# Kernel optimization log

Measured on AMD Instinct MI355X. Metric: run time of the kernel, lower is better.

## Reference

```python
import jax, jax.numpy as jnp
import numpy as np

B, D_IN, LAT, C = 16384, 512, 64, 8
HID = [1024, 512, 256]

def _lin(k, fi, fo, scale=0.02):
    k1, k2 = jax.random.split(k)
    return jax.random.normal(k1, (fi, fo), jnp.float32) * scale, jax.random.normal(k2, (fo,), jnp.float32) * scale

def _lin_c(k, fi, fo, scale=0.02):
    k1, k2 = jax.random.split(k)
    return jax.random.normal(k1, (C, fi, fo), jnp.float32) * scale, jax.random.normal(k2, (C, fo), jnp.float32) * scale

def setup_inputs() -> dict:
    key = jax.random.key(0)
    ks = jax.random.split(key, 16)
    x = jax.random.normal(ks[0], (B, D_IN), jnp.float32)
    cluster_labels = jax.random.randint(ks[1], (B,), 0, C, jnp.int32)
    eps = jax.random.normal(ks[2], (B, LAT), jnp.float32)
    # encoder: shared(512->1024), unshared(1024->512), shared(512->256)
    enc_W0, enc_b0 = _lin(ks[3], D_IN, HID[0])
    enc_Wu, enc_bu = _lin_c(ks[4], HID[0], HID[1])
    enc_W2, enc_b2 = _lin(ks[5], HID[1], HID[2])
    # shared latent heads
    mu_W, mu_b = _lin(ks[6], HID[2], LAT)
    lv_W, lv_b = _lin(ks[7], HID[2], LAT)
    # decoder (hidden_dims reversed = [256,512,1024]): unshared(64->256), shared(256->512), unshared(512->1024)
    dec_Wu0, dec_bu0 = _lin_c(ks[8], LAT, HID[2])
    dec_W1, dec_b1 = _lin(ks[9], HID[2], HID[1])
    dec_Wu2, dec_bu2 = _lin_c(ks[10], HID[1], HID[0])
    # per-cluster final layer (1024 -> input_dim), no activation (all-continuous)
    fin_W, fin_b = _lin_c(ks[11], HID[0], D_IN)
    return dict(x=x, cluster_labels=cluster_labels, eps=eps,
                enc_W0=enc_W0, enc_b0=enc_b0, enc_Wu=enc_Wu, enc_bu=enc_bu,
                enc_W2=enc_W2, enc_b2=enc_b2, mu_W=mu_W, mu_b=mu_b,
                lv_W=lv_W, lv_b=lv_b, dec_Wu0=dec_Wu0, dec_bu0=dec_bu0,
                dec_W1=dec_W1, dec_b1=dec_b1, dec_Wu2=dec_Wu2, dec_bu2=dec_bu2,
                fin_W=fin_W, fin_b=fin_b)

def _unshared(h, W, b, labels):
    # per-cluster GEMM then row-wise combine (mask-based dispatch, no row reorder)
    y = jnp.einsum('bi,cio->bco', h, W) + b[None]  # [B, C, out]
    return jnp.take_along_axis(y, labels[:, None, None], axis=1)[:, 0, :]

def reference(x, cluster_labels, eps,
              enc_W0, enc_b0, enc_Wu, enc_bu, enc_W2, enc_b2,
              mu_W, mu_b, lv_W, lv_b,
              dec_Wu0, dec_bu0, dec_W1, dec_b1, dec_Wu2, dec_bu2,
              fin_W, fin_b):
    lbl = cluster_labels.astype(jnp.int32)
    # encoder
    h = jax.nn.relu(x @ enc_W0 + enc_b0)
    h = jax.nn.relu(_unshared(h, enc_Wu, enc_bu, lbl))
    h = jax.nn.relu(h @ enc_W2 + enc_b2)
    mu = h @ mu_W + mu_b
    logvar = h @ lv_W + lv_b
    # reparameterize
    z = mu + jnp.exp(0.5 * logvar) * eps
    # decoder
    h = jax.nn.relu(_unshared(z, dec_Wu0, dec_bu0, lbl))
    h = jax.nn.relu(h @ dec_W1 + dec_b1)
    h = jax.nn.relu(_unshared(h, dec_Wu2, dec_bu2, lbl))
    # per-cluster final output layer (identity activation: all-continuous)
    recon = _unshared(h, fin_W, fin_b, lbl)
    return recon
```

## Files before the change

kernel.cpp:

```cpp
#include <hip/hip_runtime.h>

typedef _Float16 f16;
typedef __attribute__((ext_vector_type(8))) _Float16 f16x8;
typedef __attribute__((ext_vector_type(4))) _Float16 f16x4;
typedef __attribute__((ext_vector_type(4))) float    f32x4;

#define B_ROWS 16384
#define MPAD   17408
#define MTILES 136
#define NBLK   64

typedef __attribute__((address_space(1))) void as1_void;
typedef __attribute__((address_space(3))) void as3_void;

__device__ __forceinline__ void gl_lds16(const void* g, void* l) {
    __builtin_amdgcn_global_load_lds((const as1_void*)g, (as3_void*)l, 16, 0, 0);
}


__global__ __launch_bounds__(256) void k_prep(const int* __restrict__ lbl, int* __restrict__ blockhist,
                                              int* __restrict__ rowmap,
                                              const float* __restrict__ mb_, const float* __restrict__ lb_,
                                              float* __restrict__ bz, f16* __restrict__ zerob) {
    int b = blockIdx.x, t = threadIdx.x;
    int i = b * 256 + t;
    rowmap[i] = -1;
    if (b < NBLK) {
        __shared__ int h[8];
        if (t < 8) h[t] = 0;
        __syncthreads();
        atomicAdd(&h[lbl[i]], 1);
        __syncthreads();
        if (t < 8) blockhist[b * 8 + t] = h[t];
    } else if (b == NBLK) {
        if (t < 64) zerob[t] = (f16)0.f;
        if (t < 64) bz[t] = mb_[t];
        else if (t < 128) bz[t] = lb_[t - 64];
    }
}

__global__ void k_offsets(const int* __restrict__ blockhist, int* offs, int* tilec, int* blockbase) {
    __shared__ int tot[8];
    __shared__ int so[9];
    int t = threadIdx.x;
    if (t < 8) {
        int s = 0;
        for (int b = 0; b < NBLK; ++b) s += blockhist[b * 8 + t];
        tot[t] = s;
    }
    __syncthreads();
    if (t == 0) {
        int o = 0;
        for (int c = 0; c < 8; ++c) { so[c] = o; o += (tot[c] + 127) & ~127; }
        so[8] = o;
        for (int c = 0; c < 9; ++c) offs[c] = so[c];
    }
    __syncthreads();
    if (t < 8) {
        int run = so[t];
        for (int b = 0; b < NBLK; ++b) {
            blockbase[b * 8 + t] = run;
            run += blockhist[b * 8 + t];
        }
    }
    if (t < MTILES) {
        int row = t * 128, c = 7;
        for (int cc = 0; cc < 8; ++cc)
            if (row >= so[cc] && row < so[cc + 1]) c = cc;
        tilec[t] = c;
    }
}

__global__ __launch_bounds__(256) void k_scatter(const int* __restrict__ lbl,
                                                 const int* __restrict__ blockbase,
                                                 int* __restrict__ rowmap) {
    __shared__ int cur[8];
    if (threadIdx.x < 8) cur[threadIdx.x] = blockbase[blockIdx.x * 8 + threadIdx.x];
    __syncthreads();
    int i = blockIdx.x * 256 + threadIdx.x;
    int c = lbl[i];
    int pos = atomicAdd(&cur[c], 1);
    rowmap[pos] = i;
}


struct Seg { const float* s; f16* d; int K, N, b0, nx, ny; long sCS, dCS; };
struct SegTab { Seg g[10]; };

__global__ __launch_bounds__(256) void k_trans(SegTab tab, const float* __restrict__ x, f16* __restrict__ xh) {
    int bid = blockIdx.x;
    if (bid < tab.g[1].b0) {
        int i = bid * 256 + threadIdx.x;
        float4 v = ((const float4*)x)[i];
        f16x4 o = {(f16)v.x, (f16)v.y, (f16)v.z, (f16)v.w};
        ((f16x4*)xh)[i] = o;
        return;
    }
    int s = 9;
    while (bid < tab.g[s].b0) --s;
    Seg sg = tab.g[s];
    int lb = bid - sg.b0;
    int nxy = sg.nx * sg.ny;
    int z = lb / nxy; int r = lb - z * nxy;
    int by = r / sg.nx; int bx = r - by * sg.nx;
    const float* src = sg.s + (size_t)z * sg.sCS;
    f16* dst = sg.d + (size_t)z * sg.dCS;
    int n0 = bx * 32, k0 = by * 32;
    int tx = threadIdx.x & 31, ty = threadIdx.x >> 5;
    __shared__ float t[32][33];
    #pragma unroll
    for (int i = 0; i < 32; i += 8)
        t[ty + i][tx] = src[(size_t)(k0 + ty + i) * sg.N + n0 + tx];
    __syncthreads();
    #pragma unroll
    for (int i = 0; i < 32; i += 8)
        dst[(size_t)(n0 + ty + i) * sg.K + k0 + tx] = (f16)t[tx][ty + i];
}

__global__ __launch_bounds__(256) void k_reparam(const f16* __restrict__ muv, const float* __restrict__ eps,
                                                 const int* __restrict__ rowmap, f16* __restrict__ z) {
    int i = blockIdx.x * 256 + threadIdx.x;
    int p = i >> 6, j = i & 63;
    int g = rowmap[p];
    float e  = (g >= 0) ? eps[(size_t)g * 64 + j] : 0.f;
    float mu = (float)muv[(size_t)p * 128 + j];
    float lv = (float)muv[(size_t)p * 128 + 64 + j];
    z[i] = (f16)(mu + expf(0.5f * lv) * e);
}


template<int GATHER, int PERW, int RELU, int SCATTER>
__global__ __launch_bounds__(256) void gemm_k(
    const f16* __restrict__ A, const f16* __restrict__ Wt,
    const float* __restrict__ bias, f16* __restrict__ Out, float* __restrict__ OutF,
    const int* __restrict__ rowmap, const int* __restrict__ tilec,
    const f16* __restrict__ zerobuf, int K, int N)
{
    __shared__ __align__(16) f16 lA[128 * 64];
    __shared__ __align__(16) f16 lB[128 * 64];
    const int tid  = threadIdx.x;
    const int wave = tid >> 6;
    const int lane = tid & 63;

    const int id  = blockIdx.x;
    const int xcd = id & 7;
    const int jj  = id >> 3;
    const int tm  = (jj % 17) * 8 + xcd;
    const int tn  = jj / 17;
    const int r0 = tm * 128, n0 = tn * 128;

    const f16* wb = Wt;
    const float* bb = bias;
    if (PERW) {
        int c = tilec[tm];
        wb += (size_t)c * K * N;
        bb += (size_t)c * N;
    }

    const int srow = tid >> 3;
    const int sg   = tid & 7;
    const int xk16 = (sg ^ (srow & 7)) * 16;
    const size_t rowB = (size_t)K * 2;
    const size_t passB = 32 * rowB;

    const char* pa[4]; size_t stepA[4];
    #pragma unroll
    for (int p = 0; p < 4; ++p) {
        int gr = r0 + p * 32 + srow;
        if (GATHER) {
            int g = rowmap[gr];
            if (g >= 0) { pa[p] = (const char*)(A + (size_t)g * K) + xk16; stepA[p] = 128; }
            else        { pa[p] = (const char*)zerobuf;                    stepA[p] = 0;   }
        } else {
            pa[p] = (const char*)(A + (size_t)gr * K) + xk16; stepA[p] = 128;
        }
    }
    const char* pb = (const char*)(wb + (size_t)(n0 + srow) * K) + xk16;

    const int mb = (wave >> 1) * 64;
    const int nb = (wave & 1) * 64;
    const int quad = lane >> 4;
    const int r16  = lane & 15;
    const int key  = r16 & 7;

    f32x4 acc[4][4];
    #pragma unroll
    for (int i = 0; i < 4; ++i)
        #pragma unroll
        for (int j = 0; j < 4; ++j)
            acc[i][j] = (f32x4){0.f, 0.f, 0.f, 0.f};

    const int nk = K >> 6;
    for (int kb = 0; kb < nk; ++kb) {
        #pragma unroll
        for (int p = 0; p < 4; ++p)
            gl_lds16(pa[p], (char*)lA + p * 4096 + wave * 1024);
        #pragma unroll
        for (int p = 0; p < 4; ++p)
            gl_lds16(pb + p * passB, (char*)lB + p * 4096 + wave * 1024);
        __syncthreads();
        #pragma unroll
        for (int kk = 0; kk < 2; ++kk) {
            const int off = ((kk * 4 + quad) ^ key) * 16;
            f16x8 af[4], bf[4];
            #pragma unroll
            for (int i = 0; i < 4; ++i)
                af[i] = *(const f16x8*)((const char*)lA + (mb + i * 16 + r16) * 128 + off);
            #pragma unroll
            for (int j = 0; j < 4; ++j)
                bf[j] = *(const f16x8*)((const char*)lB + (nb + j * 16 + r16) * 128 + off);
            #pragma unroll
            for (int i = 0; i < 4; ++i)
                #pragma unroll
                for (int j = 0; j < 4; ++j)
                    acc[i][j] = __builtin_amdgcn_mfma_f32_16x16x32_f16(af[i], bf[j], acc[i][j], 0, 0, 0);
        }
        __syncthreads();
        #pragma unroll
        for (int p = 0; p < 4; ++p) pa[p] += stepA[p];
        pb += 128;
    }

    float bv[4];
    #pragma unroll
    for (int j = 0; j < 4; ++j) bv[j] = bb[n0 + nb + j * 16 + r16];

    #pragma unroll
    for (int i = 0; i < 4; ++i) {
        #pragma unroll
        for (int r = 0; r < 4; ++r) {
            int orow = r0 + mb + i * 16 + quad * 4 + r;
            int g = 0;
            if (SCATTER) g = rowmap[orow];
            #pragma unroll
            for (int j = 0; j < 4; ++j) {
                int ocol = n0 + nb + j * 16 + r16;
                float v = acc[i][j][r] + bv[j];
                if (RELU) v = fmaxf(v, 0.f);
                if (SCATTER) {
                    if (g >= 0) OutF[(size_t)g * N + ocol] = v;
                } else {
                    Out[(size_t)orow * N + ocol] = (f16)v;
                }
            }
        }
    }
}


extern "C" void kernel_launch(void* const* d_in, const int* in_sizes, int n_in,
                              void* d_out, int out_size, void* d_ws, size_t ws_size,
                              hipStream_t stream) {
    const float* x      = (const float*)d_in[0];
    const int*   lbl    = (const int*)  d_in[1];
    const float* eps    = (const float*)d_in[2];
    const float* enc_W0 = (const float*)d_in[3];
    const float* enc_b0 = (const float*)d_in[4];
    const float* enc_Wu = (const float*)d_in[5];
    const float* enc_bu = (const float*)d_in[6];
    const float* enc_W2 = (const float*)d_in[7];
    const float* enc_b2 = (const float*)d_in[8];
    const float* mu_W   = (const float*)d_in[9];
    const float* mu_b   = (const float*)d_in[10];
    const float* lv_W   = (const float*)d_in[11];
    const float* lv_b   = (const float*)d_in[12];
    const float* dWu0   = (const float*)d_in[13];
    const float* dbu0   = (const float*)d_in[14];
    const float* dW1    = (const float*)d_in[15];
    const float* db1    = (const float*)d_in[16];
    const float* dWu2   = (const float*)d_in[17];
    const float* dbu2   = (const float*)d_in[18];
    const float* finW   = (const float*)d_in[19];
    const float* finb   = (const float*)d_in[20];
    float* out = (float*)d_out;
    (void)in_sizes; (void)n_in; (void)out_size; (void)ws_size;

    char* base = (char*)d_ws;
    size_t off = 0;
    auto alloc = [&](size_t bytes) { char* r = base + off; off = (off + bytes + 255) & ~(size_t)255; return r; };
    f16* xh     = (f16*)alloc((size_t)B_ROWS * 512 * 2);
    f16* buf1   = (f16*)alloc((size_t)MPAD * 1024 * 2);
    f16* buf2   = (f16*)alloc((size_t)MPAD * 512 * 2);
    f16* buf3   = (f16*)alloc((size_t)MPAD * 256 * 2);
    f16* muv    = (f16*)alloc((size_t)MPAD * 128 * 2);
    f16* zb     = (f16*)alloc((size_t)MPAD * 64 * 2);
    f16* w0t    = (f16*)alloc(1024ul * 512 * 2);
    f16* wut    = (f16*)alloc(8ul * 512 * 1024 * 2);
    f16* w2t    = (f16*)alloc(256ul * 512 * 2);
    f16* wzt    = (f16*)alloc(128ul * 256 * 2);
    f16* wd0t   = (f16*)alloc(8ul * 256 * 64 * 2);
    f16* wd1t   = (f16*)alloc(512ul * 256 * 2);
    f16* wd2t   = (f16*)alloc(8ul * 1024 * 512 * 2);
    f16* wft    = (f16*)alloc(8ul * 512 * 1024 * 2);
    float* bz   = (float*)alloc(128 * 4);
    int* rowmap = (int*)alloc(MPAD * 4);
    int* blockhist = (int*)alloc(NBLK * 8 * 4);
    int* blockbase = (int*)alloc(NBLK * 8 * 4);
    int* offs   = (int*)alloc(64);
    int* tilec  = (int*)alloc(MTILES * 4);
    f16* zerob  = (f16*)alloc(256);

    k_prep<<<MPAD / 256, 256, 0, stream>>>(lbl, blockhist, rowmap, mu_b, lv_b, bz, zerob);
    k_offsets<<<1, 256, 0, stream>>>(blockhist, offs, tilec, blockbase);
    k_scatter<<<NBLK, 256, 0, stream>>>(lbl, blockbase, rowmap);

    SegTab tab;
    int b0 = B_ROWS * 512 / 4 / 256;
    auto seg = [&](int i, const float* s, f16* d, int K, int N, int nz, long sCS, long dCS) {
        int nx = N / 32, ny = K / 32;
        tab.g[i] = Seg{s, d, K, N, b0, nx, ny, sCS, dCS};
        b0 += nx * ny * nz;
    };
    tab.g[0] = Seg{nullptr, nullptr, 0, 0, 0, 0, 0, 0, 0};
    seg(1, enc_W0, w0t, 512, 1024, 1, 0, 0);
    seg(2, enc_Wu, wut, 1024, 512, 8, 1024l * 512, 512l * 1024);
    seg(3, enc_W2, w2t, 512, 256, 1, 0, 0);
    seg(4, mu_W, wzt, 256, 64, 1, 0, 0);
    seg(5, lv_W, wzt + 64 * 256, 256, 64, 1, 0, 0);
    seg(6, dWu0, wd0t, 64, 256, 8, 64l * 256, 256l * 64);
    seg(7, dW1, wd1t, 256, 512, 1, 0, 0);
    seg(8, dWu2, wd2t, 512, 1024, 8, 512l * 1024, 1024l * 512);
    seg(9, finW, wft, 1024, 512, 8, 1024l * 512, 512l * 1024);
    k_trans<<<b0, 256, 0, stream>>>(tab, x, xh);

    gemm_k<1,0,1,0><<<MTILES * 8, 256, 0, stream>>>(xh,   w0t,  enc_b0, buf1, nullptr, rowmap, tilec, zerob, 512, 1024);
    gemm_k<0,1,1,0><<<MTILES * 4, 256, 0, stream>>>(buf1, wut,  enc_bu, buf2, nullptr, rowmap, tilec, zerob, 1024, 512);
    gemm_k<0,0,1,0><<<MTILES * 2, 256, 0, stream>>>(buf2, w2t,  enc_b2, buf3, nullptr, rowmap, tilec, zerob, 512, 256);
    gemm_k<0,0,0,0><<<MTILES * 1, 256, 0, stream>>>(buf3, wzt,  bz,     muv,  nullptr, rowmap, tilec, zerob, 256, 128);
    k_reparam<<<MPAD * 64 / 256, 256, 0, stream>>>(muv, eps, rowmap, zb);
    gemm_k<0,1,1,0><<<MTILES * 2, 256, 0, stream>>>(zb,   wd0t, dbu0,   buf3, nullptr, rowmap, tilec, zerob, 64, 256);
    gemm_k<0,0,1,0><<<MTILES * 4, 256, 0, stream>>>(buf3, wd1t, db1,    buf2, nullptr, rowmap, tilec, zerob, 256, 512);
    gemm_k<0,1,1,0><<<MTILES * 8, 256, 0, stream>>>(buf2, wd2t, dbu2,   buf1, nullptr, rowmap, tilec, zerob, 512, 1024);
    gemm_k<0,1,0,1><<<MTILES * 4, 256, 0, stream>>>(buf1, wft,  finb,   nullptr, out,  rowmap, tilec, zerob, 1024, 512);
}
```

Baseline: 354.3 us.

## Stage GEMM epilogues through LDS for vectorized stores and fuse reparameterization

The GEMM epilogue now writes the accumulator tile into swizzled shared memory and then emits wide 16-byte coalesced stores, replacing per-element scattered 2-byte or 4-byte writes. The final scatter layer stages fp32 halves through LDS and writes each output row with float4 stores. The mu/logvar GEMM now computes z = mu + exp(0.5*logvar)*eps in its epilogue, which removes the separate reparam kernel and the muv buffer round trip. The cost is extra LDS traffic and synchronizations in every GEMM epilogue, and the 32 KB shared block is reused across phases.

```diff
diff --git a/kernel.cpp b/kernel.cpp
--- a/kernel.cpp
+++ b/kernel.cpp
@@ -117,27 +117,18 @@
         dst[(size_t)(n0 + ty + i) * sg.K + k0 + tx] = (f16)t[tx][ty + i];
 }
 
-__global__ __launch_bounds__(256) void k_reparam(const f16* __restrict__ muv, const float* __restrict__ eps,
-                                                 const int* __restrict__ rowmap, f16* __restrict__ z) {
-    int i = blockIdx.x * 256 + threadIdx.x;
-    int p = i >> 6, j = i & 63;
-    int g = rowmap[p];
-    float e  = (g >= 0) ? eps[(size_t)g * 64 + j] : 0.f;
-    float mu = (float)muv[(size_t)p * 128 + j];
-    float lv = (float)muv[(size_t)p * 128 + 64 + j];
-    z[i] = (f16)(mu + expf(0.5f * lv) * e);
-}
-
-
-template<int GATHER, int PERW, int RELU, int SCATTER>
+
+template<int GATHER, int PERW, int RELU, int EPI>
 __global__ __launch_bounds__(256) void gemm_k(
     const f16* __restrict__ A, const f16* __restrict__ Wt,
     const float* __restrict__ bias, f16* __restrict__ Out, float* __restrict__ OutF,
+    const float* __restrict__ eps,
     const int* __restrict__ rowmap, const int* __restrict__ tilec,
     const f16* __restrict__ zerobuf, int K, int N)
 {
-    __shared__ __align__(16) f16 lA[128 * 64];
-    __shared__ __align__(16) f16 lB[128 * 64];
+    __shared__ __align__(16) char smem[32768];
+    char* lA = smem;
+    char* lB = smem + 16384;
     const int tid  = threadIdx.x;
     const int wave = tid >> 6;
     const int lane = tid & 63;
@@ -194,10 +185,10 @@
     for (int kb = 0; kb < nk; ++kb) {
         #pragma unroll
         for (int p = 0; p < 4; ++p)
-            gl_lds16(pa[p], (char*)lA + p * 4096 + wave * 1024);
+            gl_lds16(pa[p], lA + p * 4096 + wave * 1024);
         #pragma unroll
         for (int p = 0; p < 4; ++p)
-            gl_lds16(pb + p * passB, (char*)lB + p * 4096 + wave * 1024);
+            gl_lds16(pb + p * passB, lB + p * 4096 + wave * 1024);
         __syncthreads();
         #pragma unroll
         for (int kk = 0; kk < 2; ++kk) {
@@ -205,10 +196,10 @@
             f16x8 af[4], bf[4];
             #pragma unroll
             for (int i = 0; i < 4; ++i)
-                af[i] = *(const f16x8*)((const char*)lA + (mb + i * 16 + r16) * 128 + off);
+                af[i] = *(const f16x8*)(lA + (mb + i * 16 + r16) * 128 + off);
             #pragma unroll
             for (int j = 0; j < 4; ++j)
-                bf[j] = *(const f16x8*)((const char*)lB + (nb + j * 16 + r16) * 128 + off);
+                bf[j] = *(const f16x8*)(lB + (nb + j * 16 + r16) * 128 + off);
             #pragma unroll
             for (int i = 0; i < 4; ++i)
                 #pragma unroll
@@ -225,24 +216,75 @@
     #pragma unroll
     for (int j = 0; j < 4; ++j) bv[j] = bb[n0 + nb + j * 16 + r16];
 
+    if (EPI == 1) {
+        #pragma unroll
+        for (int p = 0; p < 2; ++p) {
+            if ((mb >> 6) == p) {
+                #pragma unroll
+                for (int i = 0; i < 4; ++i) {
+                    #pragma unroll
+                    for (int r = 0; r < 4; ++r) {
+                        int lr2 = i * 16 + quad * 4 + r;
+                        #pragma unroll
+                        for (int j = 0; j < 4; ++j) {
+                            int lc = nb + j * 16 + r16;
+                            float v = acc[i][j][r] + bv[j];
+                            if (RELU) v = fmaxf(v, 0.f);
+                            *(float*)(smem + lr2 * 512 + ((((lc >> 2) ^ (lr2 & 7))) << 4) + ((lc & 3) << 2)) = v;
+                        }
+                    }
+                }
+            }
+            __syncthreads();
+            #pragma unroll
+            for (int k = 0; k < 8; ++k) {
+                int f = k * 256 + tid;
+                int row2 = f >> 5, g5 = f & 31;
+                int grow = rowmap[r0 + p * 64 + row2];
+                f32x4 vv = *(const f32x4*)(smem + row2 * 512 + (((g5 ^ (row2 & 7))) << 4));
+                if (grow >= 0)
+                    *(f32x4*)(OutF + (size_t)grow * N + n0 + g5 * 4) = vv;
+            }
+            __syncthreads();
+        }
+        return;
+    }
+
     #pragma unroll
     for (int i = 0; i < 4; ++i) {
         #pragma unroll
         for (int r = 0; r < 4; ++r) {
-            int orow = r0 + mb + i * 16 + quad * 4 + r;
-            int g = 0;
-            if (SCATTER) g = rowmap[orow];
+            int lr = mb + i * 16 + quad * 4 + r;
             #pragma unroll
             for (int j = 0; j < 4; ++j) {
-                int ocol = n0 + nb + j * 16 + r16;
+                int lc = nb + j * 16 + r16;
                 float v = acc[i][j][r] + bv[j];
                 if (RELU) v = fmaxf(v, 0.f);
-                if (SCATTER) {
-                    if (g >= 0) OutF[(size_t)g * N + ocol] = v;
-                } else {
-                    Out[(size_t)orow * N + ocol] = (f16)v;
-                }
+                *(f16*)(smem + lr * 256 + ((((lc >> 3) ^ (lr & 7))) << 4) + ((lc & 7) << 1)) = (f16)v;
             }
+        }
+    }
+    __syncthreads();
+
+    if (EPI == 0) {
+        #pragma unroll
+        for (int k = 0; k < 8; ++k) {
+            int f = k * 256 + tid;
+            int row = f >> 4, g4 = f & 15;
+            f16x8 vv = *(const f16x8*)(smem + row * 256 + (((g4 ^ (row & 7))) << 4));
+            *(f16x8*)(Out + (size_t)(r0 + row) * N + n0 + g4 * 8) = vv;
+        }
+    } else {
+        const int col = tid & 63;
+        const int rb  = tid >> 6;
+        for (int rr = 0; rr < 32; ++rr) {
+            int row = rb * 32 + rr;
+            int g = rowmap[r0 + row];
+            float e = (g >= 0) ? eps[(size_t)g * 64 + col] : 0.f;
+            float mu = (float)*(const f16*)(smem + row * 256 + ((((col >> 3) ^ (row & 7))) << 4) + ((col & 7) << 1));
+            int c2 = col + 64;
+            float lv = (float)*(const f16*)(smem + row * 256 + ((((c2 >> 3) ^ (row & 7))) << 4) + ((c2 & 7) << 1));
+            Out[(size_t)(r0 + row) * 64 + col] = (f16)(mu + expf(0.5f * lv) * e);
         }
     }
 }
@@ -282,7 +324,6 @@
     f16* buf1   = (f16*)alloc((size_t)MPAD * 1024 * 2);
     f16* buf2   = (f16*)alloc((size_t)MPAD * 512 * 2);
     f16* buf3   = (f16*)alloc((size_t)MPAD * 256 * 2);
-    f16* muv    = (f16*)alloc((size_t)MPAD * 128 * 2);
     f16* zb     = (f16*)alloc((size_t)MPAD * 64 * 2);
     f16* w0t    = (f16*)alloc(1024ul * 512 * 2);
     f16* wut    = (f16*)alloc(8ul * 512 * 1024 * 2);
@@ -323,13 +364,12 @@
     seg(9, finW, wft, 1024, 512, 8, 1024l * 512, 512l * 1024);
     k_trans<<<b0, 256, 0, stream>>>(tab, x, xh);
 
-    gemm_k<1,0,1,0><<<MTILES * 8, 256, 0, stream>>>(xh,   w0t,  enc_b0, buf1, nullptr, rowmap, tilec, zerob, 512, 1024);
-    gemm_k<0,1,1,0><<<MTILES * 4, 256, 0, stream>>>(buf1, wut,  enc_bu, buf2, nullptr, rowmap, tilec, zerob, 1024, 512);
-    gemm_k<0,0,1,0><<<MTILES * 2, 256, 0, stream>>>(buf2, w2t,  enc_b2, buf3, nullptr, rowmap, tilec, zerob, 512, 256);
-    gemm_k<0,0,0,0><<<MTILES * 1, 256, 0, stream>>>(buf3, wzt,  bz,     muv,  nullptr, rowmap, tilec, zerob, 256, 128);
-    k_reparam<<<MPAD * 64 / 256, 256, 0, stream>>>(muv, eps, rowmap, zb);
-    gemm_k<0,1,1,0><<<MTILES * 2, 256, 0, stream>>>(zb,   wd0t, dbu0,   buf3, nullptr, rowmap, tilec, zerob, 64, 256);
-    gemm_k<0,0,1,0><<<MTILES * 4, 256, 0, stream>>>(buf3, wd1t, db1,    buf2, nullptr, rowmap, tilec, zerob, 256, 512);
-    gemm_k<0,1,1,0><<<MTILES * 8, 256, 0, stream>>>(buf2, wd2t, dbu2,   buf1, nullptr, rowmap, tilec, zerob, 512, 1024);
-    gemm_k<0,1,0,1><<<MTILES * 4, 256, 0, stream>>>(buf1, wft,  finb,   nullptr, out,  rowmap, tilec, zerob, 1024, 512);
-}
+    gemm_k<1,0,1,0><<<MTILES * 8, 256, 0, stream>>>(xh,   w0t,  enc_b0, buf1, nullptr, nullptr, rowmap, tilec, zerob, 512, 1024);
+    gemm_k<0,1,1,0><<<MTILES * 4, 256, 0, stream>>>(buf1, wut,  enc_bu, buf2, nullptr, nullptr, rowmap, tilec, zerob, 1024, 512);
+    gemm_k<0,0,1,0><<<MTILES * 2, 256, 0, stream>>>(buf2, w2t,  enc_b2, buf3, nullptr, nullptr, rowmap, tilec, zerob, 512, 256);
+    gemm_k<0,0,0,2><<<MTILES * 1, 256, 0, stream>>>(buf3, wzt,  bz,     zb,   nullptr, eps,     rowmap, tilec, zerob, 256, 128);
+    gemm_k<0,1,1,0><<<MTILES * 2, 256, 0, stream>>>(zb,   wd0t, dbu0,   buf3, nullptr, nullptr, rowmap, tilec, zerob, 64, 256);
+    gemm_k<0,0,1,0><<<MTILES * 4, 256, 0, stream>>>(buf3, wd1t, db1,    buf2, nullptr, nullptr, rowmap, tilec, zerob, 256, 512);
+    gemm_k<0,1,1,0><<<MTILES * 8, 256, 0, stream>>>(buf2, wd2t, dbu2,   buf1, nullptr, nullptr, rowmap, tilec, zerob, 512, 1024);
+    gemm_k<0,1,0,1><<<MTILES * 4, 256, 0, stream>>>(buf1, wft,  finb,   nullptr, out,  nullptr, rowmap, tilec, zerob, 1024, 512);
+}
```

Measured after the change: 384.2 us. +8.5%, slower.
